# Performance work log

Hardware: AMD Instinct MI355X
Metric: run time of the kernel (lower is better)

## Reference

```python
import jax, jax.numpy as jnp
import numpy as np

ABITS = 4
WBITS = 4
BN_EPS = 1e-5


def _ste(x, q):
    # straight-through estimator: forward q, backward identity
    return x + jax.lax.stop_gradient(q - x)


def act_quant(x):
    # unsigned activation quantization to ABITS (clipped-ReLU style, as in NIPQ quantized act)
    levels = (1 << ABITS) - 1  # 15
    xc = jnp.clip(x, 0.0, 1.0)
    q = jnp.round(xc * levels) / levels
    return _ste(xc, q)


def weight_quant(w):
    # symmetric per-tensor weight quantization to WBITS
    n = (1 << (WBITS - 1)) - 1  # 7
    alpha = jnp.max(jnp.abs(w)) + 1e-12
    wc = jnp.clip(w / alpha, -1.0, 1.0)
    q = jnp.round(wc * n) / n * alpha
    return _ste(w, q)


def conv3x3(x, w):
    # NCHW, OIHW, stride 1, padding 1
    return jax.lax.conv_general_dilated(
        x, w, window_strides=(1, 1), padding=((1, 1), (1, 1)),
        dimension_numbers=('NCHW', 'OIHW', 'NCHW'))


def batchnorm(x, gamma, beta):
    # training-mode BN: batch statistics over (N,H,W)
    mean = jnp.mean(x, axis=(0, 2, 3), keepdims=True)
    var = jnp.var(x, axis=(0, 2, 3), keepdims=True)
    xhat = (x - mean) * jax.lax.rsqrt(var + BN_EPS)
    return xhat * gamma[None, :, None, None] + beta[None, :, None, None]


def setup_inputs() -> dict:
    key = jax.random.key(0)
    k = jax.random.split(key, 3)
    C = 128
    x = jax.random.normal(k[0], (64, C, 56, 56), dtype=jnp.float32)
    w1 = jax.random.normal(k[1], (C, C, 3, 3), dtype=jnp.float32) * 0.05
    w2 = jax.random.normal(k[2], (C, C, 3, 3), dtype=jnp.float32) * 0.05
    return {
        'x': x, 'w1': w1, 'w2': w2,
        'gamma1': jnp.ones((C,), jnp.float32), 'beta1': jnp.zeros((C,), jnp.float32),
        'gamma2': jnp.ones((C,), jnp.float32), 'beta2': jnp.zeros((C,), jnp.float32),
    }


def reference(x, w1, w2, gamma1, beta1, gamma2, beta2):
    identity = x
    out = act_quant(x)
    out = conv3x3(out, weight_quant(w1))
    out = batchnorm(out, gamma1, beta1)
    out = act_quant(out)
    out = conv3x3(out, weight_quant(w2))
    out = batchnorm(out, gamma2, beta2)
    return out + identity
```

## Files before the change

### kernel.cpp

```cpp
#include <hip/hip_runtime.h>

#define CH    128
#define IMG   56
#define PADW  58
#define HWSZ  3136
#define NPIX  200704
#define WELEMS 147456
#define BNEPS 1e-5f
#define PADB  430592
#define YOFF  27557888u
#define Y2OFF_B 51380224u
#define WQ1OFF_B 78938112u

typedef float f32x4 __attribute__((ext_vector_type(4)));
typedef int   i32x4 __attribute__((ext_vector_type(4)));
typedef short short8 __attribute__((ext_vector_type(8)));
typedef _Float16 f16;

__device__ __forceinline__ void async16(const void* g, void* l) {
  __builtin_amdgcn_global_load_lds(
      (const __attribute__((address_space(1))) unsigned int*)g,
      (__attribute__((address_space(3))) unsigned int*)l, 16, 0, 0);
}
__device__ __forceinline__ void bn_inline(int lin, const float* stats, const unsigned* abits,
                                          const float* g, const float* b, float* bnpS) {
  if (lin < 128) {
    const float inv = 1.f / (float)NPIX;
    float gs   = (__uint_as_float(*abits) + 1e-12f) * (1.f / 105.f);
    float mean = stats[lin] * inv;
    float var  = fmaxf(stats[CH + lin] * inv - mean * mean, 0.f);
    float sc   = g[lin] * gs * rsqrtf(gs * gs * var + BNEPS);
    bnpS[lin]      = sc;
    bnpS[CH + lin] = b[lin] - sc * mean;
  }
}
__device__ __forceinline__ void halo_zero(unsigned char* qb, int lin) {
  for (int i = lin; i < 1824; i += 256) {
    size_t off;
    if (i < 464)      off = (size_t)i * 16;
    else if (i < 928) off = (size_t)57 * PADW * 128 + (size_t)(i - 464) * 16;
    else {
      int j = i - 928, loc = j >> 3, sub = j & 7;
      int row = 1 + (loc >> 1), col = (loc & 1) ? 57 : 0;
      off = ((size_t)row * PADW + col) * 128 + (size_t)sub * 16;
    }
    *(uint4*)(qb + off) = (uint4){0u, 0u, 0u, 0u};
  }
}

__global__ void k_wmax(const float* __restrict__ w1, const float* __restrict__ w2,
                       unsigned* __restrict__ alpha_bits) {
  int idx = blockIdx.x * 256 + threadIdx.x;
  float m1 = 0.f, m2 = 0.f;
  for (int i = idx; i < WELEMS; i += gridDim.x * 256) {
    m1 = fmaxf(m1, fabsf(w1[i]));
    m2 = fmaxf(m2, fabsf(w2[i]));
  }
#pragma unroll
  for (int off = 32; off > 0; off >>= 1) {
    m1 = fmaxf(m1, __shfl_xor(m1, off));
    m2 = fmaxf(m2, __shfl_xor(m2, off));
  }
  __shared__ float s1[4], s2[4];
  int wave = threadIdx.x >> 6;
  if ((threadIdx.x & 63) == 0) { s1[wave] = m1; s2[wave] = m2; }
  __syncthreads();
  if (threadIdx.x == 0) {
    m1 = fmaxf(fmaxf(s1[0], s1[1]), fmaxf(s1[2], s1[3]));
    m2 = fmaxf(fmaxf(s2[0], s2[1]), fmaxf(s2[2], s2[3]));
    atomicMax(&alpha_bits[0], __float_as_uint(m1));
    atomicMax(&alpha_bits[1], __float_as_uint(m2));
  }
}

__global__ void k_wquant(const float* __restrict__ w1, const float* __restrict__ w2,
                         const unsigned* __restrict__ alpha_bits,
                         unsigned char* __restrict__ wq1, unsigned char* __restrict__ wq2) {
  int idx = blockIdx.x * 256 + threadIdx.x;
  int t = idx >= WELEMS;
  int j = t ? idx - WELEMS : idx;
  int kk  = j >> 14;
  int rem = j & 16383;
  int co = rem >> 7, ci = rem & 127;
  float alpha = __uint_as_float(alpha_bits[t]) + 1e-12f;
  float v  = (t ? w2 : w1)[co * 1152 + ci * 9 + kk];
  float wc = fminf(fmaxf(v / alpha, -1.f), 1.f);
  int q = (int)rintf(wc * 7.f);
  (t ? wq2 : wq1)[j] = (unsigned char)(q & 0xFF);
}

__global__ void k_actq(const float* __restrict__ x, unsigned char* __restrict__ qx) {
  __shared__ float tile[32][33];
  int n = blockIdx.z, p0 = blockIdx.x * 32, c0 = blockIdx.y * 32;
  int tx = threadIdx.x, ty = threadIdx.y, lin = ty * 32 + tx;
  unsigned char* qb = qx + (size_t)n * PADB;
  if (blockIdx.x == 0 && blockIdx.y == 0) halo_zero(qb, lin);
  const float* xs = x + ((size_t)n * CH + c0) * HWSZ;
#pragma unroll
  for (int r = 0; r < 4; ++r) {
    int c = ty + r * 8;
    float v = xs[(size_t)c * HWSZ + p0 + tx];
    v = fminf(fmaxf(v, 0.f), 1.f);
    tile[c][tx] = rintf(v * 15.f);
  }
  __syncthreads();
#pragma unroll
  for (int r = 0; r < 4; ++r) {
    int pl = p0 + ty + r * 8;
    int h = pl / IMG, w = pl - h * IMG;
    qb[((h + 1) * PADW + (w + 1)) * 128 + c0 + tx] = (unsigned char)(int)tile[tx][ty + r * 8];
  }
}

#define CONV_SETUP(PCALC)                                                        \
  const int tid  = threadIdx.x;                                                  \
  const int lane = tid & 63;                                                     \
  const int quad = lane >> 4, lrow = lane & 15;                                  \
  const int m_off = ((tid >> 6) >> 1) * 64, n_off = ((tid >> 6) & 1) * 64;       \
  const unsigned char* asrc[4]; int boff[4], ldsoff[4];                          \
  _Pragma("unroll")                                                              \
  for (int i = 0; i < 4; ++i) {                                                  \
    int c = i * 256 + tid;                                                       \
    int r = c >> 3;                                                              \
    int srccol = ((c & 7) ^ (r & 7)) * 16;          \
    ldsoff[i] = (i * 256 + (tid & ~63)) * 16;                                    \
    PCALC                                                                        \
    boff[i] = r * 128 + srccol;                                                  \
  }                                                                              \
  int acol[2];                                                                   \
  _Pragma("unroll")                                                              \
  for (int j = 0; j < 2; ++j)                                                    \
    acol[j] = ((4 * j + quad) ^ (lrow & 7)) << 4;                                \
  i32x4 acc[4][4];                                                               \
  _Pragma("unroll")                                                              \
  for (int mi = 0; mi < 4; ++mi)                                                 \
    _Pragma("unroll")                                                            \
    for (int ni = 0; ni < 4; ++ni) acc[mi][ni] = (i32x4){0, 0, 0, 0};

#define PCALC_GLOBAL                                                             \
    int p = blockIdx.x * 128 + r;                                                \
    int n = p / HWSZ, l = p - n * HWSZ;                                          \
    int h = l / IMG, w = l - h * IMG;                                            \
    asrc[i] = act + (size_t)n * PADB + ((h + 1) * PADW + (w + 1)) * 128 + srccol;

#define PCALC_IMG                                                                \
    int p = blockIdx.x * 128 + r;                                                \
    if (p > HWSZ - 1) p = HWSZ - 1;              \
    int h = p / IMG, w = p - h * IMG;                                            \
    asrc[i] = act + ((h + 1) * PADW + (w + 1)) * 128 + srccol;

#define CONV_KLOOP(WQ)                                                           \
  {                 \
    _Pragma("unroll")                                                            \
    for (int i = 0; i < 4; ++i) async16(asrc[i] - (PADW + 1) * 128, smem + ldsoff[i]); \
    _Pragma("unroll")                                                            \
    for (int i = 0; i < 4; ++i) async16((WQ) + boff[i], smem + 16384 + ldsoff[i]); \
    __syncthreads();                                                             \
  }                                                                              \
  for (int kk = 0; kk < 9; ++kk) {                                               \
    if (kk < 8) {                      \
      const int kn = kk + 1;                                                     \
      const int doff = ((kn / 3 - 1) * PADW + (kn % 3 - 1)) * 128;               \
      char* nb = smem + ((kn & 1) << 15);                                        \
      _Pragma("unroll")                                                          \
      for (int i = 0; i < 4; ++i) async16(asrc[i] + doff, nb + ldsoff[i]);       \
      _Pragma("unroll")                                                          \
      for (int i = 0; i < 4; ++i) async16((WQ) + kn * 16384 + boff[i], nb + 16384 + ldsoff[i]); \
    }                                                                            \
    const char* As = smem + ((kk & 1) << 15);                                    \
    const char* Bs = As + 16384;                                                 \
    __builtin_amdgcn_s_setprio(1);                                               \
    _Pragma("unroll")                                                            \
    for (int j = 0; j < 2; ++j) {                                                \
      i32x4 af[4], bf[4];                                                        \
      _Pragma("unroll")                                                          \
      for (int mi = 0; mi < 4; ++mi)                                             \
        af[mi] = *(const i32x4*)(As + (m_off + mi * 16 + lrow) * 128 + acol[j]); \
      _Pragma("unroll")                                                          \
      for (int ni = 0; ni < 4; ++ni)                                             \
        bf[ni] = *(const i32x4*)(Bs + (n_off + ni * 16 + lrow) * 128 + acol[j]); \
      _Pragma("unroll")                                                          \
      for (int mi = 0; mi < 4; ++mi)                                             \
        _Pragma("unroll")                                                        \
        for (int ni = 0; ni < 4; ++ni)                                           \
          acc[mi][ni] = __builtin_amdgcn_mfma_i32_16x16x64_i8(af[mi], bf[ni], acc[mi][ni], 0, 0, 0); \
    }                                                                            \
    __builtin_amdgcn_s_setprio(0);                                               \
    __syncthreads();     \
  }

__global__ __launch_bounds__(256, 2)
void k_conv(const unsigned char* __restrict__ act, const unsigned char* __restrict__ wq,
            short* __restrict__ y, float* __restrict__ stats) {
  __shared__ __align__(16) char smem[66560];
  CONV_SETUP(PCALC_GLOBAL)
  CONV_KLOOP(wq)
  float lsum[4] = {0.f, 0.f, 0.f, 0.f}, lsq[4] = {0.f, 0.f, 0.f, 0.f};
#pragma unroll
  for (int mi = 0; mi < 4; ++mi) {
    int prow = blockIdx.x * 128 + m_off + mi * 16 + quad * 4;
#pragma unroll
    for (int ni = 0; ni < 4; ++ni) {
      int co = n_off + ni * 16 + lrow;
#pragma unroll
      for (int rg = 0; rg < 4; ++rg) {
        float v = (float)acc[mi][ni][rg];
        y[(size_t)(prow + rg) * CH + co] = (short)fminf(fmaxf(v, -32767.f), 32767.f);
        lsum[ni] += v; lsq[ni] += v * v;
      }
    }
  }
#pragma unroll
  for (int ni = 0; ni < 4; ++ni) {
    lsum[ni] += __shfl_xor(lsum[ni], 16); lsum[ni] += __shfl_xor(lsum[ni], 32);
    lsq[ni]  += __shfl_xor(lsq[ni], 16);  lsq[ni]  += __shfl_xor(lsq[ni], 32);
  }
  __syncthreads();
  float* red = (float*)(smem + 65536);
  red[tid] = 0.f;
  __syncthreads();
  if (quad == 0) {
#pragma unroll
    for (int ni = 0; ni < 4; ++ni) {
      int co = n_off + ni * 16 + lrow;
      atomicAdd(&red[co], lsum[ni]);
      atomicAdd(&red[CH + co], lsq[ni]);
    }
  }
  __syncthreads();
  atomicAdd(&stats[tid], red[tid]);
}

__global__ void k_bnq(const short* __restrict__ y, const float* __restrict__ stats,
                      const unsigned* __restrict__ abits, const float* __restrict__ g,
                      const float* __restrict__ b, unsigned char* __restrict__ q) {
  __shared__ float bnpS[256];
  int tid = threadIdx.x;
  bn_inline(tid, stats, abits, g, b, bnpS);
  if (blockIdx.x < 64) halo_zero(q + (size_t)blockIdx.x * PADB, tid);
  __syncthreads();
  size_t i = (size_t)blockIdx.x * 256 + tid;
  short8 v = ((const short8*)y)[i];
  int c0 = (int)((i * 8) & (CH - 1));
  int pix = (int)(i >> 4);
  int n = pix / HWSZ, l = pix - n * HWSZ;
  int h = l / IMG, w = l - h * IMG;
  unsigned lo = 0u, hi = 0u;
#pragma unroll
  for (int j = 0; j < 8; ++j) {
    float u = (float)v[j] * bnpS[c0 + j] + bnpS[CH + c0 + j];
    unsigned qv = (unsigned)(int)rintf(fminf(fmaxf(u, 0.f), 1.f) * 15.f);
    if (j < 4) lo |= qv << (8 * j); else hi |= qv << (8 * (j - 4));
  }
  *(uint2*)(q + (size_t)n * PADB + ((h + 1) * PADW + (w + 1)) * 128 + c0) =
      (uint2){lo, hi};
}

__global__ void k_fin(const short* __restrict__ y2, const float* __restrict__ stats,
                      const unsigned* __restrict__ abits, const float* __restrict__ g,
                      const float* __restrict__ b, const float* __restrict__ x,
                      float* __restrict__ out, int img0) {
  __shared__ float bnpS[256];
  __shared__ float tile[32][33];
  int tx = threadIdx.x, ty = threadIdx.y, lin = ty * 32 + tx;
  bn_inline(lin, stats, abits, g, b, bnpS);
  __syncthreads();
  int n = img0 + blockIdx.z, p0 = blockIdx.x * 32, c0 = blockIdx.y * 32;
  const short* ys = y2 + (size_t)n * HWSZ * CH;
  float sc = bnpS[c0 + tx], sh = bnpS[CH + c0 + tx];
#pragma unroll
  for (int r = 0; r < 4; ++r) {
    int p = p0 + ty + r * 8;
    tile[ty + r * 8][tx] = (float)ys[(size_t)p * CH + c0 + tx] * sc + sh;
  }
  __syncthreads();
  const float* xs = x + ((size_t)n * CH + c0) * HWSZ;
  float*       os = out + ((size_t)n * CH + c0) * HWSZ;
#pragma unroll
  for (int r = 0; r < 4; ++r) {
    int c = ty + r * 8;
    size_t a = (size_t)c * HWSZ + p0 + tx;
    os[a] = tile[tx][c] + xs[a];
  }
}

__global__ __launch_bounds__(256, 2)
void k_conv_out63(const unsigned char* __restrict__ act, const unsigned char* __restrict__ wq,
                  const float* __restrict__ stats, const unsigned* __restrict__ abits,
                  const float* __restrict__ g, const float* __restrict__ b,
                  const float* __restrict__ x, float* __restrict__ out) {
  __shared__ __align__(16) char smem[66560];
  __shared__ float bnpS[256];
  bn_inline(threadIdx.x, stats, abits, g, b, bnpS);
  CONV_SETUP(PCALC_IMG)
  CONV_KLOOP(wq)
  __syncthreads();
  f16 (*tile)[132] = (f16(*)[132])smem;
#pragma unroll
  for (int ni = 0; ni < 4; ++ni) {
    int co = n_off + ni * 16 + lrow;
    float sc = bnpS[co], sh = bnpS[CH + co];
#pragma unroll
    for (int mi = 0; mi < 4; ++mi) {
      int pr = m_off + mi * 16 + quad * 4;
#pragma unroll
      for (int rg = 0; rg < 4; ++rg)
        tile[co][pr + rg] = (f16)((float)acc[mi][ni][rg] * sc + sh);
    }
  }
  __syncthreads();
  int c = tid >> 1, seg = tid & 1;
  int pl0 = blockIdx.x * 128 + seg * 64;
  if (pl0 < HWSZ) {
    size_t gb = ((size_t)63 * CH + c) * HWSZ + pl0;
    const float* xp = x + gb;
    float* op = out + gb;
    const f16* tr = &tile[c][seg * 64];
#pragma unroll
    for (int j = 0; j < 64; j += 4) {
      f32x4 xv = *(const f32x4*)(xp + j);
      f32x4 ov;
      ov[0] = (float)tr[j]     + xv[0];
      ov[1] = (float)tr[j + 1] + xv[1];
      ov[2] = (float)tr[j + 2] + xv[2];
      ov[3] = (float)tr[j + 3] + xv[3];
      *(f32x4*)(op + j) = ov;
    }
  }
}

extern "C" void kernel_launch(void* const* d_in, const int* in_sizes, int n_in,
                              void* d_out, int out_size, void* d_ws, size_t ws_size,
                              hipStream_t stream) {
  (void)in_sizes; (void)n_in; (void)out_size;
  const float* x  = (const float*)d_in[0];
  const float* w1 = (const float*)d_in[1];
  const float* w2 = (const float*)d_in[2];
  const float* g1 = (const float*)d_in[3];
  const float* b1 = (const float*)d_in[4];
  const float* g2 = (const float*)d_in[5];
  const float* b2 = (const float*)d_in[6];
  float* out = (float*)d_out;

  char* dob = (char*)d_out;
  unsigned char* q1p = (unsigned char*)dob;
  unsigned char* q2p = (unsigned char*)dob;
  short* y1 = (short*)(dob + YOFF);

  char* ws = (char*)d_ws;
  unsigned* alpha_bits = (unsigned*)ws;
  float* stats1 = (float*)(ws + 256);
  float* stats2 = (float*)(ws + 1280);

  const bool bigws = ws_size >= 51679744u;
  unsigned char *wq1, *wq2;
  short* y2;
  if (bigws) {
    wq1 = (unsigned char*)(ws + 4608);
    wq2 = (unsigned char*)(ws + 152064);
    y2  = (short*)(ws + 299520);
  } else {
    wq1 = (unsigned char*)(dob + WQ1OFF_B);
    wq2 = (unsigned char*)(ws + 4608);
    y2  = (short*)(dob + Y2OFF_B);
  }
  unsigned char* q63p = (unsigned char*)(ws + 152064);

  hipMemsetAsync(ws, 0, 4608, stream);
  k_wmax  <<<64, 256, 0, stream>>>(w1, w2, alpha_bits);
  k_wquant<<<2 * WELEMS / 256, 256, 0, stream>>>(w1, w2, alpha_bits, wq1, wq2);
  k_actq  <<<dim3(98, 4, 64), dim3(32, 8), 0, stream>>>(x, q1p);
  k_conv  <<<NPIX / 128, 256, 0, stream>>>(q1p, wq1, y1, stats1);
  k_bnq   <<<NPIX * CH / 2048, 256, 0, stream>>>(y1, stats1, alpha_bits + 0, g1, b1, q2p);
  k_conv  <<<NPIX / 128, 256, 0, stream>>>(q2p, wq2, y2, stats2);

  if (bigws) {
    k_fin <<<dim3(98, 4, 64), dim3(32, 8), 0, stream>>>(y2, stats2, alpha_bits + 1, g2, b2, x, out, 0);
  } else {
    hipMemcpyAsync(q63p, q2p + (size_t)63 * PADB, PADB, hipMemcpyDeviceToDevice, stream);
    k_fin <<<dim3(98, 4, 32), dim3(32, 8), 0, stream>>>(y2, stats2, alpha_bits + 1, g2, b2, x, out, 0);
    k_fin <<<dim3(98, 4, 16), dim3(32, 8), 0, stream>>>(y2, stats2, alpha_bits + 1, g2, b2, x, out, 32);
    k_fin <<<dim3(98, 4,  8), dim3(32, 8), 0, stream>>>(y2, stats2, alpha_bits + 1, g2, b2, x, out, 48);
    k_fin <<<dim3(98, 4,  4), dim3(32, 8), 0, stream>>>(y2, stats2, alpha_bits + 1, g2, b2, x, out, 56);
    k_fin <<<dim3(98, 4,  2), dim3(32, 8), 0, stream>>>(y2, stats2, alpha_bits + 1, g2, b2, x, out, 60);
    k_fin <<<dim3(98, 4,  1), dim3(32, 8), 0, stream>>>(y2, stats2, alpha_bits + 1, g2, b2, x, out, 62);
    k_conv_out63<<<25, 256, 0, stream>>>(q63p, wq2, stats2, alpha_bits + 1, g2, b2, x, out);
  }
}
```

Measured before the change: 370.5 us.

## Stage padded input strip once per block and reuse it across all nine taps

The implicit-GEMM conv now has each block cover 4 image rows (224 pixels). Each block loads the padded 6-row activation strip into LDS once, and the 9 kernel taps read shifted windows from that strip. Before, a fresh 128-pixel A tile was reloaded for every tap. Only the weight tiles stay double-buffered per tap. This cuts redundant global/LDS traffic for activations and raises the per-wave MFMA tile to 7x4, at the cost of more accumulator registers (112 int32) and more LDS, which may reduce occupancy under launch_bounds(256,2).

```diff
diff --git a/kernel.cpp b/kernel.cpp
--- a/kernel.cpp
+++ b/kernel.cpp
@@ -11,6 +11,14 @@
 #define YOFF  27557888u
 #define Y2OFF_B 51380224u
 #define WQ1OFF_B 78938112u
+
+#define BPIX   224
+#define NBLK   (NPIX / BPIX)
+#define STRIPB 44544
+#define STRIPC 2784
+#define BBASE  44544
+#define REDOFF 77312
+#define SMEMSZ 78336
 
 typedef float f32x4 __attribute__((ext_vector_type(4)));
 typedef int   i32x4 __attribute__((ext_vector_type(4)));
@@ -112,96 +120,103 @@
   }
 }
 
-#define CONV_SETUP(PCALC)                                                        \
+#define CONV_SETUP2                                                              \
   const int tid  = threadIdx.x;                                                  \
   const int lane = tid & 63;                                                     \
   const int quad = lane >> 4, lrow = lane & 15;                                  \
-  const int m_off = ((tid >> 6) >> 1) * 64, n_off = ((tid >> 6) & 1) * 64;       \
-  const unsigned char* asrc[4]; int boff[4], ldsoff[4];                          \
+  const int m_base = ((tid >> 6) >> 1) * 112, n_base = ((tid >> 6) & 1) * 64;    \
+  int sbase[7];                                                                  \
+  _Pragma("unroll")                                                              \
+  for (int mi = 0; mi < 7; ++mi) {                                               \
+    int row = m_base + mi * 16 + lrow;                                           \
+    sbase[mi] = (row / 56) * 58 + (row % 56);                                    \
+  }                                                                              \
+  int boff[4], bldsoff[4];                                                       \
   _Pragma("unroll")                                                              \
   for (int i = 0; i < 4; ++i) {                                                  \
     int c = i * 256 + tid;                                                       \
     int r = c >> 3;                                                              \
-    int srccol = ((c & 7) ^ (r & 7)) * 16;          \
-    ldsoff[i] = (i * 256 + (tid & ~63)) * 16;                                    \
-    PCALC                                                                        \
-    boff[i] = r * 128 + srccol;                                                  \
+    boff[i] = r * 128 + ((c & 7) ^ (r & 7)) * 16;                                \
+    bldsoff[i] = (i * 256 + (tid & ~63)) * 16;                                   \
   }                                                                              \
-  int acol[2];                                                                   \
-  _Pragma("unroll")                                                              \
-  for (int j = 0; j < 2; ++j)                                                    \
-    acol[j] = ((4 * j + quad) ^ (lrow & 7)) << 4;                                \
-  i32x4 acc[4][4];                                                               \
-  _Pragma("unroll")                                                              \
-  for (int mi = 0; mi < 4; ++mi)                                                 \
+  i32x4 acc[7][4];                                                               \
+  _Pragma("unroll")                                                              \
+  for (int mi = 0; mi < 7; ++mi)                                                 \
     _Pragma("unroll")                                                            \
     for (int ni = 0; ni < 4; ++ni) acc[mi][ni] = (i32x4){0, 0, 0, 0};
 
-#define PCALC_GLOBAL                                                             \
-    int p = blockIdx.x * 128 + r;                                                \
-    int n = p / HWSZ, l = p - n * HWSZ;                                          \
-    int h = l / IMG, w = l - h * IMG;                                            \
-    asrc[i] = act + (size_t)n * PADB + ((h + 1) * PADW + (w + 1)) * 128 + srccol;
-
-#define PCALC_IMG                                                                \
-    int p = blockIdx.x * 128 + r;                                                \
-    if (p > HWSZ - 1) p = HWSZ - 1;              \
-    int h = p / IMG, w = p - h * IMG;                                            \
-    asrc[i] = act + ((h + 1) * PADW + (w + 1)) * 128 + srccol;
-
-#define CONV_KLOOP(WQ)                                                           \
-  {                 \
+#define CONV_STAGE_PRO(STRIPSRC, WQ)                                             \
+  _Pragma("unroll")                                                              \
+  for (int it = 0; it < 11; ++it) {                                              \
+    int u = it * 256 + tid;                                                      \
+    if (u < STRIPC) {                                                            \
+      int s = u >> 3, cc = u & 7;                                                \
+      async16((STRIPSRC) + s * 128 + ((cc ^ (s & 7)) << 4),                      \
+              smem + (it * 256 + (tid & ~63)) * 16);                             \
+    }                                                                            \
+  }                                                                              \
+  _Pragma("unroll")                                                              \
+  for (int i = 0; i < 4; ++i) async16((WQ) + boff[i], smem + BBASE + bldsoff[i]);\
+  __syncthreads();
+
+#define CONV_KLOOP2(WQ)                                                          \
+  _Pragma("unroll")                                                              \
+  for (int kk = 0; kk < 9; ++kk) {                                               \
+    if (kk < 8) {                                 \
+      const int kn = kk + 1;                                                     \
+      char* nb = smem + BBASE + ((kn & 1) << 14);                                \
+      _Pragma("unroll")                                                          \
+      for (int i = 0; i < 4; ++i)                                                \
+        async16((WQ) + kn * 16384 + boff[i], nb + bldsoff[i]);                   \
+    }                                                                            \
+    const char* Bs = smem + BBASE + ((kk & 1) << 14);                            \
+    const int dkk = (kk / 3) * 58 + (kk % 3);                                    \
+    int aaddr[7];                                                                \
     _Pragma("unroll")                                                            \
-    for (int i = 0; i < 4; ++i) async16(asrc[i] - (PADW + 1) * 128, smem + ldsoff[i]); \
-    _Pragma("unroll")                                                            \
-    for (int i = 0; i < 4; ++i) async16((WQ) + boff[i], smem + 16384 + ldsoff[i]); \
-    __syncthreads();                                                             \
-  }                                                                              \
-  for (int kk = 0; kk < 9; ++kk) {                                               \
-    if (kk < 8) {                      \
-      const int kn = kk + 1;                                                     \
-      const int doff = ((kn / 3 - 1) * PADW + (kn % 3 - 1)) * 128;               \
-      char* nb = smem + ((kn & 1) << 15);                                        \
-      _Pragma("unroll")                                                          \
-      for (int i = 0; i < 4; ++i) async16(asrc[i] + doff, nb + ldsoff[i]);       \
-      _Pragma("unroll")                                                          \
-      for (int i = 0; i < 4; ++i) async16((WQ) + kn * 16384 + boff[i], nb + 16384 + ldsoff[i]); \
+    for (int mi = 0; mi < 7; ++mi) {                                             \
+      int s = sbase[mi] + dkk;                                                   \
+      aaddr[mi] = (s << 7) + ((quad << 4) ^ ((s & 7) << 4));                     \
     }                                                                            \
-    const char* As = smem + ((kk & 1) << 15);                                    \
-    const char* Bs = As + 16384;                                                 \
     __builtin_amdgcn_s_setprio(1);                                               \
     _Pragma("unroll")                                                            \
     for (int j = 0; j < 2; ++j) {                                                \
-      i32x4 af[4], bf[4];                                                        \
+      i32x4 af[7], bf[4];                                                        \
       _Pragma("unroll")                                                          \
-      for (int mi = 0; mi < 4; ++mi)                                             \
-        af[mi] = *(const i32x4*)(As + (m_off + mi * 16 + lrow) * 128 + acol[j]); \
+      for (int mi = 0; mi < 7; ++mi)                                             \
+        af[mi] = *(const i32x4*)(smem + (aaddr[mi] ^ (j << 6)));                 \
       _Pragma("unroll")                                                          \
-      for (int ni = 0; ni < 4; ++ni)                                             \
-        bf[ni] = *(const i32x4*)(Bs + (n_off + ni * 16 + lrow) * 128 + acol[j]); \
+      for (int ni = 0; ni < 4; ++ni) {                                           \
+        int brow = n_base + ni * 16 + lrow;                                      \
+        bf[ni] = *(const i32x4*)(Bs + brow * 128 +                               \
+                                 (((j << 6) | (quad << 4)) ^ ((brow & 7) << 4)));\
+      }                                                                          \
       _Pragma("unroll")                                                          \
-      for (int mi = 0; mi < 4; ++mi)                                             \
+      for (int mi = 0; mi < 7; ++mi)                                             \
         _Pragma("unroll")                                                        \
         for (int ni = 0; ni < 4; ++ni)                                           \
           acc[mi][ni] = __builtin_amdgcn_mfma_i32_16x16x64_i8(af[mi], bf[ni], acc[mi][ni], 0, 0, 0); \
     }                                                                            \
     __builtin_amdgcn_s_setprio(0);                                               \
-    __syncthreads();     \
+    __syncthreads();                                                             \
   }
 
 __global__ __launch_bounds__(256, 2)
 void k_conv(const unsigned char* __restrict__ act, const unsigned char* __restrict__ wq,
             short* __restrict__ y, float* __restrict__ stats) {
-  __shared__ __align__(16) char smem[66560];
-  CONV_SETUP(PCALC_GLOBAL)
-  CONV_KLOOP(wq)
+  __shared__ __align__(16) char smem[SMEMSZ];
+  const int n = blockIdx.x / 14, br = blockIdx.x % 14;
+  const unsigned char* strip = act + (size_t)n * PADB + (size_t)br * 4 * PADW * 128;
+  CONV_SETUP2
+  CONV_STAGE_PRO(strip, wq)
+  CONV_KLOOP2(wq)
+  const int pbase = n * HWSZ + br * BPIX;
   float lsum[4] = {0.f, 0.f, 0.f, 0.f}, lsq[4] = {0.f, 0.f, 0.f, 0.f};
 #pragma unroll
-  for (int mi = 0; mi < 4; ++mi) {
-    int prow = blockIdx.x * 128 + m_off + mi * 16 + quad * 4;
+  for (int mi = 0; mi < 7; ++mi) {
+    int prow = pbase + m_base + mi * 16 + quad * 4;
 #pragma unroll
     for (int ni = 0; ni < 4; ++ni) {
-      int co = n_off + ni * 16 + lrow;
+      int co = n_base + ni * 16 + lrow;
 #pragma unroll
       for (int rg = 0; rg < 4; ++rg) {
         float v = (float)acc[mi][ni][rg];
@@ -216,13 +231,13 @@
     lsq[ni]  += __shfl_xor(lsq[ni], 16);  lsq[ni]  += __shfl_xor(lsq[ni], 32);
   }
   __syncthreads();
-  float* red = (float*)(smem + 65536);
+  float* red = (float*)(smem + REDOFF);
   red[tid] = 0.f;
   __syncthreads();
   if (quad == 0) {
 #pragma unroll
     for (int ni = 0; ni < 4; ++ni) {
-      int co = n_off + ni * 16 + lrow;
+      int co = n_base + ni * 16 + lrow;
       atomicAdd(&red[co], lsum[ni]);
       atomicAdd(&red[CH + co], lsq[ni]);
     }
@@ -289,20 +304,23 @@
                   const float* __restrict__ stats, const unsigned* __restrict__ abits,
                   const float* __restrict__ g, const float* __restrict__ b,
                   const float* __restrict__ x, float* __restrict__ out) {
-  __shared__ __align__(16) char smem[66560];
+  __shared__ __align__(16) char smem[SMEMSZ];
   __shared__ float bnpS[256];
   bn_inline(threadIdx.x, stats, abits, g, b, bnpS);
-  CONV_SETUP(PCALC_IMG)
-  CONV_KLOOP(wq)
-  __syncthreads();
-  f16 (*tile)[132] = (f16(*)[132])smem;
+  const int br = blockIdx.x;
+  const unsigned char* strip = act + (size_t)br * 4 * PADW * 128;
+  CONV_SETUP2
+  CONV_STAGE_PRO(strip, wq)
+  CONV_KLOOP2(wq)
+  __syncthreads();
+  f16 (*tile)[228] = (f16(*)[228])smem;
 #pragma unroll
   for (int ni = 0; ni < 4; ++ni) {
-    int co = n_off + ni * 16 + lrow;
+    int co = n_base + ni * 16 + lrow;
     float sc = bnpS[co], sh = bnpS[CH + co];
 #pragma unroll
-    for (int mi = 0; mi < 4; ++mi) {
-      int pr = m_off + mi * 16 + quad * 4;
+    for (int mi = 0; mi < 7; ++mi) {
+      int pr = m_base + mi * 16 + quad * 4;
 #pragma unroll
       for (int rg = 0; rg < 4; ++rg)
         tile[co][pr + rg] = (f16)((float)acc[mi][ni][rg] * sc + sh);
@@ -310,22 +328,20 @@
   }
   __syncthreads();
   int c = tid >> 1, seg = tid & 1;
-  int pl0 = blockIdx.x * 128 + seg * 64;
-  if (pl0 < HWSZ) {
-    size_t gb = ((size_t)63 * CH + c) * HWSZ + pl0;
-    const float* xp = x + gb;
-    float* op = out + gb;
-    const f16* tr = &tile[c][seg * 64];
-#pragma unroll
-    for (int j = 0; j < 64; j += 4) {
-      f32x4 xv = *(const f32x4*)(xp + j);
-      f32x4 ov;
-      ov[0] = (float)tr[j]     + xv[0];
-      ov[1] = (float)tr[j + 1] + xv[1];
-      ov[2] = (float)tr[j + 2] + xv[2];
-      ov[3] = (float)tr[j + 3] + xv[3];
-      *(f32x4*)(op + j) = ov;
-    }
+  int pl0 = br * BPIX + seg * 112;
+  size_t gb = ((size_t)63 * CH + c) * HWSZ + pl0;
+  const float* xp = x + gb;
+  float* op = out + gb;
+  const f16* tr = &tile[c][seg * 112];
+#pragma unroll
+  for (int j = 0; j < 112; j += 4) {
+    f32x4 xv = *(const f32x4*)(xp + j);
+    f32x4 ov;
+    ov[0] = (float)tr[j]     + xv[0];
+    ov[1] = (float)tr[j + 1] + xv[1];
+    ov[2] = (float)tr[j + 2] + xv[2];
+    ov[3] = (float)tr[j + 3] + xv[3];
+    *(f32x4*)(op + j) = ov;
   }
 }
 
@@ -370,9 +386,9 @@
   k_wmax  <<<64, 256, 0, stream>>>(w1, w2, alpha_bits);
   k_wquant<<<2 * WELEMS / 256, 256, 0, stream>>>(w1, w2, alpha_bits, wq1, wq2);
   k_actq  <<<dim3(98, 4, 64), dim3(32, 8), 0, stream>>>(x, q1p);
-  k_conv  <<<NPIX / 128, 256, 0, stream>>>(q1p, wq1, y1, stats1);
+  k_conv  <<<NBLK, 256, 0, stream>>>(q1p, wq1, y1, stats1);
   k_bnq   <<<NPIX * CH / 2048, 256, 0, stream>>>(y1, stats1, alpha_bits + 0, g1, b1, q2p);
-  k_conv  <<<NPIX / 128, 256, 0, stream>>>(q2p, wq2, y2, stats2);
+  k_conv  <<<NBLK, 256, 0, stream>>>(q2p, wq2, y2, stats2);
 
   if (bigws) {
     k_fin <<<dim3(98, 4, 64), dim3(32, 8), 0, stream>>>(y2, stats2, alpha_bits + 1, g2, b2, x, out, 0);
@@ -384,6 +400,6 @@
     k_fin <<<dim3(98, 4,  4), dim3(32, 8), 0, stream>>>(y2, stats2, alpha_bits + 1, g2, b2, x, out, 56);
     k_fin <<<dim3(98, 4,  2), dim3(32, 8), 0, stream>>>(y2, stats2, alpha_bits + 1, g2, b2, x, out, 60);
     k_fin <<<dim3(98, 4,  1), dim3(32, 8), 0, stream>>>(y2, stats2, alpha_bits + 1, g2, b2, x, out, 62);
-    k_conv_out63<<<25, 256, 0, stream>>>(q63p, wq2, stats2, alpha_bits + 1, g2, b2, x, out);
-  }
-}
+    k_conv_out63<<<14, 256, 0, stream>>>(q63p, wq2, stats2, alpha_bits + 1, g2, b2, x, out);
+  }
+}
```

New measurement: 337.5 us. 1.1x faster.
